# Optimization experiments

Hardware: AMD Instinct MI355X
Metric: run time of the kernel (lower is better)

## Reference

```python
import jax, jax.numpy as jnp
from jax import lax
import numpy as np

BN_EPS = 1e-5

def _bn(x, g, b, m, v):
    # inference-mode BatchNorm1d (running stats)
    return (x - m) * (g / jnp.sqrt(v + BN_EPS)) + b

def _mlp2(x, W1, g, b, m, v, W2):
    # Linear(no bias) -> BN -> ReLU -> (Dropout off in eval) -> Linear(no bias)
    h = jax.nn.relu(_bn(x @ W1.T, g, b, m, v))
    return h @ W2.T

def setup_inputs() -> dict:
    key = jax.random.key(0)
    ks = iter(jax.random.split(key, 40))
    B, N = 1024, 10
    f32 = jnp.float32
    def w(shape, s=0.02):
        return jax.random.normal(next(ks), shape, f32) * s
    def bn_params(c):
        return (jnp.ones((c,), f32), jnp.zeros((c,), f32),
                jax.random.normal(next(ks), (c,), f32) * 0.1,
                jax.random.uniform(next(ks), (c,), f32, 0.5, 1.5))
    inp = {
        'features_object': jax.random.normal(next(ks), (B, N, 1024), f32),
        'bbox': jax.random.uniform(next(ks), (B, N, 4), f32),
        'word_embedding': jax.random.normal(next(ks), (B, N, 300), f32),
        'sentiment': jax.random.normal(next(ks), (B, N, 4096), f32),
        'body': jax.random.normal(next(ks), (B, 2048), f32),
    }
    # mlp_object: 1024 -> 128 -> 128
    inp['W1_o'] = w((128, 1024)); inp['g_o'], inp['b_o'], inp['m_o'], inp['v_o'] = bn_params(128)
    inp['W2_o'] = w((128, 128))
    # mlp_sentiment: 4096 -> 512 -> 128
    inp['W1_s'] = w((512, 4096)); inp['g_s'], inp['b_s'], inp['m_s'], inp['v_s'] = bn_params(512)
    inp['W2_s'] = w((128, 512))
    # mlp_body: 2048 -> 256 -> 128
    inp['W1_b'] = w((256, 2048)); inp['g_b'], inp['b_b'], inp['m_b'], inp['v_b'] = bn_params(256)
    inp['W2_b'] = w((128, 256))
    # channel attention (CBAM-style, in_planes=10, ratio=2): shared MLP 10->5->10
    inp['Wc1'] = w((5, 10), 0.3)
    inp['Wc2'] = w((10, 5), 0.3)
    # spatial attention: Conv1d(2 -> 1, k=7, pad=3, no bias)
    inp['Wsa'] = w((1, 2, 7), 0.3)
    # fc1: 688 -> 256 (with bias) then BN
    inp['Wf'] = w((256, 688)); inp['bf'] = jnp.zeros((256,), f32)
    inp['g_f'], inp['b_f'], inp['m_f'], inp['v_f'] = bn_params(256)
    return inp

def reference(features_object, bbox, word_embedding, sentiment, body,
              W1_o, g_o, b_o, m_o, v_o, W2_o,
              W1_s, g_s, b_s, m_s, v_s, W2_s,
              W1_b, g_b, b_b, m_b, v_b, W2_b,
              Wc1, Wc2, Wsa, Wf, bf, g_f, b_f, m_f, v_f):
    B, N, _ = features_object.shape
    # per-slice MLPs batched into single GEMMs over B*N rows
    obj = _mlp2(features_object.reshape(B * N, -1), W1_o, g_o, b_o, m_o, v_o, W2_o).reshape(B, N, 128)
    sen = _mlp2(sentiment.reshape(B * N, -1), W1_s, g_s, b_s, m_s, v_s, W2_s).reshape(B, N, 128)
    # body is identical across the N repeats (inference BN), compute once and broadcast
    bod = _mlp2(body.reshape(B, -1), W1_b, g_b, b_b, m_b, v_b, W2_b)
    bod = jnp.broadcast_to(bod[:, None, :], (B, N, 128))
    x = jnp.concatenate([obj, bbox, word_embedding, sen, bod], axis=2)  # [B,N,688]
    # channel attention over the N-slice axis
    def ca_mlp(a):  # [B,N] -> [B,N]
        return jax.nn.relu(a @ Wc1.T) @ Wc2.T
    att_c = jax.nn.sigmoid(ca_mlp(x.mean(axis=2)) + ca_mlp(x.max(axis=2)))  # [B,N]
    x = x * att_c[:, :, None]
    # spatial attention along feature axis
    s = jnp.stack([x.mean(axis=1), x.max(axis=1)], axis=1)  # [B,2,688]
    sa = lax.conv_general_dilated(s, Wsa, (1,), [(3, 3)],
                                  dimension_numbers=('NCH', 'OIH', 'NCH'))  # [B,1,688]
    x = x * jax.nn.sigmoid(sa)
    x = x.sum(axis=1)  # [B,688]
    out = jax.nn.relu(_bn(x @ Wf.T + bf, g_f, b_f, m_f, v_f))  # [B,256]
    return out
```

## Files before the change

### kernel.cpp

```cpp
#include <hip/hip_runtime.h>
#include <hip/hip_bf16.h>
#include <math.h>

typedef __attribute__((ext_vector_type(8))) short short8;
typedef __attribute__((ext_vector_type(4))) float floatx4;

static __device__ __forceinline__ unsigned short f2bf(float f) {
    unsigned int u = __float_as_uint(f);
    unsigned int r = (u + 0x7fffu + ((u >> 16) & 1u)) >> 16;
    return (unsigned short)r;
}

static __device__ __forceinline__ unsigned int pk_bf16(float lo, float hi) {
    unsigned int r;
    asm("v_cvt_pk_bf16_f32 %0, %1, %2" : "=v"(r) : "v"(lo), "v"(hi));
    return r;
}

static __device__ __forceinline__ void g2l16(const void* g, void* l) {
    __builtin_amdgcn_global_load_lds(
        (const __attribute__((address_space(1))) unsigned int*)g,
        (__attribute__((address_space(3))) unsigned int*)l,
        16, 0, 0);
}

static __device__ __forceinline__ float4 bnrelu4(float4 v, float4 s, float4 h) {
    float4 r;
    r.x = fmaxf(v.x * s.x + h.x, 0.f);
    r.y = fmaxf(v.y * s.y + h.y, 0.f);
    r.z = fmaxf(v.z * s.z + h.z, 0.f);
    r.w = fmaxf(v.w * s.w + h.w, 0.f);
    return r;
}

struct GDesc {
    const float*          Af;
    const unsigned short* Ab;
    const unsigned short* W;
    float*          Cf;
    unsigned short* Cb;
    const float *bias, *g, *b, *m, *v;
    int M, N, K;
    int Kreal;
    int fuse;
    int nbx;
    int block0;
    int nbb;
    int ksplit;
    int fuseA;
};
struct GArgs { GDesc g[3]; int n; };

__global__ __launch_bounds__(256)
void gemm_grouped(GArgs ga)
{
    __shared__ float          As_f[2][4096];
    __shared__ unsigned short Bs[2][4096];
    __shared__ float scL[256], shL[256];
    unsigned short* As_b = (unsigned short*)&As_f[0][0];

    const int bid = blockIdx.x;
    int gi = 0;
    #pragma unroll
    for (int i = 1; i < 3; ++i)
        if (i < ga.n && bid >= ga.g[i].block0) gi = i;
    const GDesc d = ga.g[gi];

    int local = bid - d.block0;
    {
        const int cpx = (d.nbb * d.ksplit) >> 3;
        local = (local & 7) * cpx + (local >> 3);
    }
    int kc = 0;
    int Kc = d.K;
    if (d.ksplit > 1) {
        Kc = d.K / d.ksplit;
        kc = local / d.nbb;
        local -= kc * d.nbb;
    }
    const int kbeg = kc * Kc;
    const int bx = local % d.nbx;
    const int by = local / d.nbx;
    const int row0 = by * 128;
    const int col0 = bx * 128;

    const int tid  = threadIdx.x;
    const int wave = tid >> 6;
    const int lane = tid & 63;
    const int qd   = lane >> 4;
    const int ln   = lane & 15;
    const int wr   = (wave >> 1) * 64;
    const int wc   = (wave & 1) * 64;

    const int c0 = wave * 128 + lane;
    const int c1 = c0 + 64;
    const int r0 = c0 >> 2, k0 = (((c0 & 3) ^ ((c0 >> 3) & 3))) * 8;
    const int r1 = c1 >> 2, k1 = (((c1 & 3) ^ ((c1 >> 3) & 3))) * 8;

    const int aro  = wave * 32 + (lane >> 3);
    const int acol = ((lane & 7) ^ (lane >> 3)) * 4;

    const bool afp = (d.Af != nullptr);
    const int niter = Kc >> 5;

    floatx4 acc[4][4];
    #pragma unroll
    for (int i = 0; i < 4; ++i)
        #pragma unroll
        for (int j = 0; j < 4; ++j) acc[i][j] = (floatx4){0.f, 0.f, 0.f, 0.f};

    if (d.fuseA) {
        for (int k = tid; k < Kc; k += 256) {
            float sc = d.g[kbeg + k] * rsqrtf(d.v[kbeg + k] + 1e-5f);
            scL[k] = sc;
            shL[k] = d.b[kbeg + k] - d.m[kbeg + k] * sc;
        }
    }
    g2l16(d.W + (size_t)(col0 + r0) * d.K + kbeg + k0, &Bs[0][(size_t)wave * 1024]);
    g2l16(d.W + (size_t)(col0 + r1) * d.K + kbeg + k1, &Bs[0][(size_t)wave * 1024 + 512]);
    if (afp) {
        #pragma unroll
        for (int t = 0; t < 4; ++t)
            g2l16(d.Af + (size_t)(row0 + aro + t * 8) * d.Kreal + kbeg + acol,
                  &As_f[0][(size_t)(wave * 4 + t) * 256]);
    } else {
        g2l16(d.Ab + (size_t)(row0 + r0) * d.K + kbeg + k0, As_b + (size_t)wave * 1024);
        g2l16(d.Ab + (size_t)(row0 + r1) * d.K + kbeg + k1, As_b + (size_t)wave * 1024 + 512);
    }
    __syncthreads();

    int cur = 0;
    for (int it = 0; it < niter; ++it) {
        const int nxt = cur ^ 1;
        const bool pf = (it + 1 < niter);

        if (pf) {
            const int kg = kbeg + (it + 1) * 32;
            g2l16(d.W + (size_t)(col0 + r0) * d.K + kg + k0, &Bs[nxt][(size_t)wave * 1024]);
            g2l16(d.W + (size_t)(col0 + r1) * d.K + kg + k1, &Bs[nxt][(size_t)wave * 1024 + 512]);
            if (afp) {
                #pragma unroll
                for (int t = 0; t < 4; ++t)
                    g2l16(d.Af + (size_t)(row0 + aro + t * 8) * d.Kreal + kg + acol,
                          &As_f[nxt][(size_t)(wave * 4 + t) * 256]);
            } else {
                g2l16(d.Ab + (size_t)(row0 + r0) * d.K + kg + k0, As_b + (size_t)nxt * 4096 + wave * 1024);
                g2l16(d.Ab + (size_t)(row0 + r1) * d.K + kg + k1, As_b + (size_t)nxt * 4096 + wave * 1024 + 512);
            }
        }

        short8 a[4], b[4];
        if (afp) {
            const int kl = it * 32;
            #pragma unroll
            for (int i = 0; i < 4; ++i) {
                const int row = wr + i * 16 + ln;
                const int sw  = row & 7;
                const int c0f = ((qd * 2)     ^ sw) * 4;
                const int c1f = ((qd * 2 + 1) ^ sw) * 4;
                float4 v0 = *(const float4*)&As_f[cur][row * 32 + c0f];
                float4 v1 = *(const float4*)&As_f[cur][row * 32 + c1f];
                if (d.fuseA) {
                    const int kf = kl + qd * 8;
                    v0 = bnrelu4(v0, *(const float4*)&scL[kf],
                                     *(const float4*)&shL[kf]);
                    v1 = bnrelu4(v1, *(const float4*)&scL[kf + 4],
                                     *(const float4*)&shL[kf + 4]);
                }
                int4 pk = { (int)pk_bf16(v0.x, v0.y), (int)pk_bf16(v0.z, v0.w),
                            (int)pk_bf16(v1.x, v1.y), (int)pk_bf16(v1.z, v1.w) };
                a[i] = *(short8*)&pk;
            }
        } else {
            #pragma unroll
            for (int i = 0; i < 4; ++i) {
                const int row = wr + i * 16 + ln;
                const int sw  = (row >> 1) & 3;
                a[i] = *(const short8*)&As_b[(size_t)cur * 4096 + row * 32 + (qd ^ sw) * 8];
            }
        }
        #pragma unroll
        for (int j = 0; j < 4; ++j) {
            const int row = wc + j * 16 + ln;
            const int sw  = (row >> 1) & 3;
            b[j] = *(const short8*)&Bs[cur][row * 32 + (qd ^ sw) * 8];
        }
        #pragma unroll
        for (int i = 0; i < 4; ++i)
            #pragma unroll
            for (int j = 0; j < 4; ++j)
                acc[i][j] = __builtin_amdgcn_mfma_f32_16x16x32_bf16(
                                a[i], b[j], acc[i][j], 0, 0, 0);

        __syncthreads();
        cur = nxt;
    }

    if (d.ksplit > 1) {
        #pragma unroll
        for (int j = 0; j < 4; ++j) {
            const int col = col0 + wc + j * 16 + ln;
            #pragma unroll
            for (int i = 0; i < 4; ++i) {
                #pragma unroll
                for (int r = 0; r < 4; ++r) {
                    const int row = row0 + wr + i * 16 + qd * 4 + r;
                    atomicAdd(&d.Cf[(size_t)row * d.N + col], acc[i][j][r]);
                }
            }
        }
        return;
    }

    #pragma unroll
    for (int j = 0; j < 4; ++j) {
        const int col = col0 + wc + j * 16 + ln;
        float add = d.bias ? d.bias[col] : 0.f;
        float scale = 1.f, shift = 0.f;
        if (d.fuse) {
            scale = d.g[col] * rsqrtf(d.v[col] + 1e-5f);
            shift = d.b[col] - d.m[col] * scale;
        }
        #pragma unroll
        for (int i = 0; i < 4; ++i) {
            #pragma unroll
            for (int r = 0; r < 4; ++r) {
                const int row = row0 + wr + i * 16 + qd * 4 + r;
                float vv = acc[i][j][r] + add;
                if (d.fuse) vv = fmaxf(vv * scale + shift, 0.f);
                if (d.Cf) d.Cf[(size_t)row * d.N + col] = vv;
                if (d.Cb) d.Cb[(size_t)row * d.N + col] = f2bf(vv);
            }
        }
    }
}

struct WSeg { const float* src; void* dst; int Kreal; int Kp; };
struct WArgs { WSeg s[7]; int off[8]; float4* zdst; int zn; };

__global__ __launch_bounds__(256)
void cvt_weights(WArgs wa)
{
    int i = blockIdx.x * 256 + threadIdx.x;
    if (i >= wa.off[7]) {
        int z = i - wa.off[7];
        if (z < wa.zn) wa.zdst[z] = (float4){0.f, 0.f, 0.f, 0.f};
        return;
    }
    int s = 0;
    #pragma unroll
    for (int j = 1; j < 7; ++j) if (i >= wa.off[j]) s = j;
    const WSeg sg = wa.s[s];
    const int li = i - wa.off[s];
    if (s == 6) {
        const int k2 = li >> 8, c = li & 255;
        const int ka = k2 * 2, kb = k2 * 2 + 1;
        unsigned int lo = (ka < 688) ? f2bf(sg.src[(size_t)c * 688 + ka]) : 0u;
        unsigned int hi = (kb < 688) ? f2bf(sg.src[(size_t)c * 688 + kb]) : 0u;
        ((unsigned int*)sg.dst)[li] = lo | (hi << 16);
        return;
    }
    const int r = li / sg.Kp, c = li - r * sg.Kp;
    ((unsigned short*)sg.dst)[li] =
        (c < sg.Kreal) ? f2bf(sg.src[(size_t)r * sg.Kreal + c]) : (unsigned short)0;
}

__global__ __launch_bounds__(256)
void attn_kernel(const float* __restrict__ obj, const float* __restrict__ bbox,
                 const float* __restrict__ word, const float* __restrict__ sen,
                 const float* __restrict__ bod,
                 const float* __restrict__ Wc1, const float* __restrict__ Wc2,
                 const float* __restrict__ Wsa,
                 const unsigned int* __restrict__ wfpk,
                 const float* __restrict__ bf,
                 const float* __restrict__ g_f, const float* __restrict__ b_f,
                 const float* __restrict__ m_f, const float* __restrict__ v_f,
                 float* __restrict__ out)
{
    const int b = blockIdx.x;
    const int tid = threadIdx.x;

    __shared__ float xs[10][688];
    __shared__ float s0[688], s1[688];
    __shared__ float xr[688];
    __shared__ float avec[10], mvec[10], att[10];
    __shared__ float cw[14], c1[50], c2[50];

    if (tid < 14) cw[tid] = Wsa[tid];
    if (tid < 50) { c1[tid] = Wc1[tid]; c2[tid] = Wc2[tid]; }

    for (int n = 0; n < 10; ++n) {
        const float* o  = obj  + ((size_t)b * 10 + n) * 128;
        const float* bx = bbox + ((size_t)b * 10 + n) * 4;
        const float* w  = word + ((size_t)b * 10 + n) * 300;
        const float* s  = sen  + ((size_t)b * 10 + n) * 128;
        const float* bo = bod  + (size_t)b * 128;
        for (int c = tid; c < 688; c += 256) {
            float v;
            if      (c < 128) v = o[c];
            else if (c < 132) v = bx[c - 128];
            else if (c < 432) v = w[c - 132];
            else if (c < 560) v = s[c - 432];
            else              v = bo[c - 560];
            xs[n][c] = v;
        }
    }
    __syncthreads();

    {
        const int wv = tid >> 6, ln2 = tid & 63;
        for (int n = wv; n < 10; n += 4) {
            float sm = 0.f, mx = -INFINITY;
            for (int c = ln2; c < 688; c += 64) {
                float v = xs[n][c];
                sm += v; mx = fmaxf(mx, v);
            }
            #pragma unroll
            for (int off = 32; off > 0; off >>= 1) {
                sm += __shfl_down(sm, off);
                mx = fmaxf(mx, __shfl_down(mx, off));
            }
            if (ln2 == 0) { avec[n] = sm * (1.f / 688.f); mvec[n] = mx; }
        }
    }
    __syncthreads();

    if (tid == 0) {
        float ha[5], hm[5];
        #pragma unroll
        for (int i = 0; i < 5; ++i) {
            float sa_ = 0.f, sm_ = 0.f;
            #pragma unroll
            for (int j = 0; j < 10; ++j) {
                sa_ += c1[i * 10 + j] * avec[j];
                sm_ += c1[i * 10 + j] * mvec[j];
            }
            ha[i] = fmaxf(sa_, 0.f);
            hm[i] = fmaxf(sm_, 0.f);
        }
        #pragma unroll
        for (int j = 0; j < 10; ++j) {
            float v = 0.f;
            #pragma unroll
            for (int i = 0; i < 5; ++i) v += c2[j * 5 + i] * (ha[i] + hm[i]);
            att[j] = 1.f / (1.f + expf(-v));
        }
    }
    __syncthreads();

    for (int c = tid; c < 688; c += 256) {
        float sm = 0.f, mx = -INFINITY;
        #pragma unroll
        for (int n = 0; n < 10; ++n) {
            float v = xs[n][c] * att[n];
            xs[n][c] = v;
            sm += v; mx = fmaxf(mx, v);
        }
        s0[c] = sm * 0.1f;
        s1[c] = mx;
    }
    __syncthreads();

    for (int c = tid; c < 688; c += 256) {
        float sa = 0.f;
        #pragma unroll
        for (int j = 0; j < 7; ++j) {
            int cc = c + j - 3;
            if (cc >= 0 && cc < 688)
                sa += cw[j] * s0[cc] + cw[7 + j] * s1[cc];
        }
        float sig = 1.f / (1.f + expf(-sa));
        float sm = 0.f;
        #pragma unroll
        for (int n = 0; n < 10; ++n) sm += xs[n][c];
        xr[c] = sm * sig;
    }
    __syncthreads();

    {
        float acc = 0.f;
        #pragma unroll 4
        for (int k2 = 0; k2 < 344; ++k2) {
            unsigned int w2 = wfpk[(size_t)k2 * 256 + tid];
            float wlo = __uint_as_float(w2 << 16);
            float whi = __uint_as_float(w2 & 0xffff0000u);
            acc += wlo * xr[2 * k2] + whi * xr[2 * k2 + 1];
        }
        float sc = g_f[tid] * rsqrtf(v_f[tid] + 1e-5f);
        float sh = b_f[tid] - m_f[tid] * sc;
        out[(size_t)b * 256 + tid] = fmaxf((acc + bf[tid]) * sc + sh, 0.f);
    }
}

extern "C" void kernel_launch(void* const* d_in, const int* in_sizes, int n_in,
                              void* d_out, int out_size, void* d_ws, size_t ws_size,
                              hipStream_t stream)
{
    const float* f_obj = (const float*)d_in[0];
    const float* bbox  = (const float*)d_in[1];
    const float* word  = (const float*)d_in[2];
    const float* sent  = (const float*)d_in[3];
    const float* body  = (const float*)d_in[4];
    const float* W1_o  = (const float*)d_in[5];
    const float* g_o = (const float*)d_in[6],  *b_o = (const float*)d_in[7];
    const float* m_o = (const float*)d_in[8],  *v_o = (const float*)d_in[9];
    const float* W2_o  = (const float*)d_in[10];
    const float* W1_s  = (const float*)d_in[11];
    const float* g_s = (const float*)d_in[12], *b_s = (const float*)d_in[13];
    const float* m_s = (const float*)d_in[14], *v_s = (const float*)d_in[15];
    const float* W2_s  = (const float*)d_in[16];
    const float* W1_b  = (const float*)d_in[17];
    const float* g_b = (const float*)d_in[18], *b_b = (const float*)d_in[19];
    const float* m_b = (const float*)d_in[20], *v_b = (const float*)d_in[21];
    const float* W2_b  = (const float*)d_in[22];
    const float* Wc1 = (const float*)d_in[23];
    const float* Wc2 = (const float*)d_in[24];
    const float* Wsa = (const float*)d_in[25];
    const float* Wf  = (const float*)d_in[26];
    const float* bf  = (const float*)d_in[27];
    const float* g_f = (const float*)d_in[28], *b_f = (const float*)d_in[29];
    const float* m_f = (const float*)d_in[30], *v_f = (const float*)d_in[31];
    float* out = (float*)d_out;

    char* p = (char*)d_ws;
    unsigned short* w1s  = (unsigned short*)p; p += 4194304;
    unsigned short* w2s  = (unsigned short*)p; p += 131072;
    unsigned short* w1o  = (unsigned short*)p; p += 262144;
    unsigned short* w2o  = (unsigned short*)p; p += 32768;
    unsigned short* w1b  = (unsigned short*)p; p += 1048576;
    unsigned short* w2b  = (unsigned short*)p; p += 65536;
    unsigned int*   wfpk = (unsigned int*)p;   p += 360448;
    char* zbase = p;
    float* sen_f = (float*)p; p += 5242880;
    float* obj_f = (float*)p; p += 5242880;
    float* bod_f = (float*)p; p += 524288;
    float* ps    = (float*)p; p += 20971520;
    float* po    = (float*)p; p += 5242880;
    float* pb    = (float*)p; p += 1048576;
    const int zbytes = 38273024;
    if ((size_t)(p - (char*)d_ws) > ws_size) return;

    WArgs wa;
    wa.s[0] = { W1_s, w1s,  4096, 4096 };
    wa.s[1] = { W2_s, w2s,   512,  512 };
    wa.s[2] = { W1_o, w1o,  1024, 1024 };
    wa.s[3] = { W2_o, w2o,   128,  128 };
    wa.s[4] = { W1_b, w1b,  2048, 2048 };
    wa.s[5] = { W2_b, w2b,   256,  256 };
    wa.s[6] = { Wf,   wfpk,  688,  704 };
    const int wn[7] = { 512*4096, 128*512, 128*1024, 128*128, 256*2048, 128*256, 352*256 };
    wa.off[0] = 0;
    for (int i = 0; i < 7; ++i) wa.off[i + 1] = wa.off[i] + wn[i];
    wa.zdst = (float4*)zbase;
    wa.zn   = zbytes / 16;
    cvt_weights<<<(wa.off[7] + wa.zn + 255) / 256, 256, 0, stream>>>(wa);

    {
        GArgs ga; ga.n = 3;
        ga.g[0] = { sent,  nullptr, w1s, ps, nullptr, nullptr, nullptr, nullptr, nullptr, nullptr,
                    10240, 512, 4096, 4096, 0, 4, 0,   320, 2, 0 };
        ga.g[1] = { f_obj, nullptr, w1o, po, nullptr, nullptr, nullptr, nullptr, nullptr, nullptr,
                    10240, 128, 1024, 1024, 0, 1, 640, 80,  2, 0 };
        ga.g[2] = { body,  nullptr, w1b, pb, nullptr, nullptr, nullptr, nullptr, nullptr, nullptr,
                    1024,  256, 2048, 2048, 0, 2, 800, 16,  2, 0 };
        gemm_grouped<<<832, 256, 0, stream>>>(ga);
    }

    {
        GArgs ga; ga.n = 3;
        ga.g[0] = { ps, nullptr, w2s, sen_f, nullptr, nullptr, g_s, b_s, m_s, v_s,
                    10240, 128, 512, 512, 0, 1, 0,   80, 2, 1 };
        ga.g[1] = { po, nullptr, w2o, obj_f, nullptr, nullptr, g_o, b_o, m_o, v_o,
                    10240, 128, 128, 128, 0, 1, 160, 80, 2, 1 };
        ga.g[2] = { pb, nullptr, w2b, bod_f, nullptr, nullptr, g_b, b_b, m_b, v_b,
                    1024,  128, 256, 256, 0, 1, 320, 8,  2, 1 };
        gemm_grouped<<<336, 256, 0, stream>>>(ga);
    }

    attn_kernel<<<1024, 256, 0, stream>>>(obj_f, bbox, word, sen_f, bod_f,
                                          Wc1, Wc2, Wsa, wfpk, bf,
                                          g_f, b_f, m_f, v_f, out);
}
```

Baseline: 495.5 us.

## Fuse second MLP layers with BN/ReLU into attention kernel

The second-layer GEMMs for the sentiment, object and body branches, with their BN+ReLU on the hidden activations, move into the per-batch attention kernel. There they run as scalar FMA loops over packed bf16 weights and bf16 hidden values held in shared memory. This removes one grouped GEMM launch and the fp32 intermediate round-trip (sen_f/obj_f/bod_f), and shrinks the zeroed workspace. In exchange the attention kernel does about 128x(512+128) MACs per row on CUDA cores instead of MFMA, and its shared-memory use rises, which may lower occupancy. The GEMM kernel is simplified to the split-K atomic path only.

Measured after the change: 561.6 us. +13.3%, slower.

```diff
diff --git a/kernel.cpp b/kernel.cpp
--- a/kernel.cpp
+++ b/kernel.cpp
@@ -24,30 +24,16 @@
         16, 0, 0);
 }
 
-static __device__ __forceinline__ float4 bnrelu4(float4 v, float4 s, float4 h) {
-    float4 r;
-    r.x = fmaxf(v.x * s.x + h.x, 0.f);
-    r.y = fmaxf(v.y * s.y + h.y, 0.f);
-    r.z = fmaxf(v.z * s.z + h.z, 0.f);
-    r.w = fmaxf(v.w * s.w + h.w, 0.f);
-    return r;
-}
-
 struct GDesc {
     const float*          Af;
-    const unsigned short* Ab;
     const unsigned short* W;
     float*          Cf;
-    unsigned short* Cb;
-    const float *bias, *g, *b, *m, *v;
     int M, N, K;
     int Kreal;
-    int fuse;
     int nbx;
     int block0;
     int nbb;
     int ksplit;
-    int fuseA;
 };
 struct GArgs { GDesc g[3]; int n; };
 
@@ -56,8 +42,6 @@
 {
     __shared__ float          As_f[2][4096];
     __shared__ unsigned short Bs[2][4096];
-    __shared__ float scL[256], shL[256];
-    unsigned short* As_b = (unsigned short*)&As_f[0][0];
 
     const int bid = blockIdx.x;
     int gi = 0;
@@ -100,7 +84,6 @@
     const int aro  = wave * 32 + (lane >> 3);
     const int acol = ((lane & 7) ^ (lane >> 3)) * 4;
 
-    const bool afp = (d.Af != nullptr);
     const int niter = Kc >> 5;
 
     floatx4 acc[4][4];
@@ -109,24 +92,12 @@
         #pragma unroll
         for (int j = 0; j < 4; ++j) acc[i][j] = (floatx4){0.f, 0.f, 0.f, 0.f};
 
-    if (d.fuseA) {
-        for (int k = tid; k < Kc; k += 256) {
-            float sc = d.g[kbeg + k] * rsqrtf(d.v[kbeg + k] + 1e-5f);
-            scL[k] = sc;
-            shL[k] = d.b[kbeg + k] - d.m[kbeg + k] * sc;
-        }
-    }
     g2l16(d.W + (size_t)(col0 + r0) * d.K + kbeg + k0, &Bs[0][(size_t)wave * 1024]);
     g2l16(d.W + (size_t)(col0 + r1) * d.K + kbeg + k1, &Bs[0][(size_t)wave * 1024 + 512]);
-    if (afp) {
-        #pragma unroll
-        for (int t = 0; t < 4; ++t)
-            g2l16(d.Af + (size_t)(row0 + aro + t * 8) * d.Kreal + kbeg + acol,
-                  &As_f[0][(size_t)(wave * 4 + t) * 256]);
-    } else {
-        g2l16(d.Ab + (size_t)(row0 + r0) * d.K + kbeg + k0, As_b + (size_t)wave * 1024);
-        g2l16(d.Ab + (size_t)(row0 + r1) * d.K + kbeg + k1, As_b + (size_t)wave * 1024 + 512);
-    }
+    #pragma unroll
+    for (int t = 0; t < 4; ++t)
+        g2l16(d.Af + (size_t)(row0 + aro + t * 8) * d.Kreal + kbeg + acol,
+              &As_f[0][(size_t)(wave * 4 + t) * 256]);
     __syncthreads();
 
     int cur = 0;
@@ -138,46 +109,22 @@
             const int kg = kbeg + (it + 1) * 32;
             g2l16(d.W + (size_t)(col0 + r0) * d.K + kg + k0, &Bs[nxt][(size_t)wave * 1024]);
             g2l16(d.W + (size_t)(col0 + r1) * d.K + kg + k1, &Bs[nxt][(size_t)wave * 1024 + 512]);
-            if (afp) {
-                #pragma unroll
-                for (int t = 0; t < 4; ++t)
-                    g2l16(d.Af + (size_t)(row0 + aro + t * 8) * d.Kreal + kg + acol,
-                          &As_f[nxt][(size_t)(wave * 4 + t) * 256]);
-            } else {
-                g2l16(d.Ab + (size_t)(row0 + r0) * d.K + kg + k0, As_b + (size_t)nxt * 4096 + wave * 1024);
-                g2l16(d.Ab + (size_t)(row0 + r1) * d.K + kg + k1, As_b + (size_t)nxt * 4096 + wave * 1024 + 512);
-            }
+            #pragma unroll
+            for (int t = 0; t < 4; ++t)
+                g2l16(d.Af + (size_t)(row0 + aro + t * 8) * d.Kreal + kg + acol,
+                      &As_f[nxt][(size_t)(wave * 4 + t) * 256]);
         }
 
         short8 a[4], b[4];
-        if (afp) {
-            const int kl = it * 32;
-            #pragma unroll
-            for (int i = 0; i < 4; ++i) {
-                const int row = wr + i * 16 + ln;
-                const int sw  = row & 7;
-                const int c0f = ((qd * 2)     ^ sw) * 4;
-                const int c1f = ((qd * 2 + 1) ^ sw) * 4;
-                float4 v0 = *(const float4*)&As_f[cur][row * 32 + c0f];
-                float4 v1 = *(const float4*)&As_f[cur][row * 32 + c1f];
-                if (d.fuseA) {
-                    const int kf = kl + qd * 8;
-                    v0 = bnrelu4(v0, *(const float4*)&scL[kf],
-                                     *(const float4*)&shL[kf]);
-                    v1 = bnrelu4(v1, *(const float4*)&scL[kf + 4],
-                                     *(const float4*)&shL[kf + 4]);
-                }
-                int4 pk = { (int)pk_bf16(v0.x, v0.y), (int)pk_bf16(v0.z, v0.w),
-                            (int)pk_bf16(v1.x, v1.y), (int)pk_bf16(v1.z, v1.w) };
-                a[i] = *(short8*)&pk;
-            }
-        } else {
-            #pragma unroll
-            for (int i = 0; i < 4; ++i) {
-                const int row = wr + i * 16 + ln;
-                const int sw  = (row >> 1) & 3;
-                a[i] = *(const short8*)&As_b[(size_t)cur * 4096 + row * 32 + (qd ^ sw) * 8];
-            }
+        #pragma unroll
+        for (int i = 0; i < 4; ++i) {
+            const int row = wr + i * 16 + ln;
+            const int sw  = row & 7;
+            float4 v0 = *(const float4*)&As_f[cur][row * 32 + ((qd * 2)     ^ sw) * 4];
+            float4 v1 = *(const float4*)&As_f[cur][row * 32 + ((qd * 2 + 1) ^ sw) * 4];
+            int4 pk = { (int)pk_bf16(v0.x, v0.y), (int)pk_bf16(v0.z, v0.w),
+                        (int)pk_bf16(v1.x, v1.y), (int)pk_bf16(v1.z, v1.w) };
+            a[i] = *(short8*)&pk;
         }
         #pragma unroll
         for (int j = 0; j < 4; ++j) {
@@ -196,46 +143,21 @@
         cur = nxt;
     }
 
-    if (d.ksplit > 1) {
-        #pragma unroll
-        for (int j = 0; j < 4; ++j) {
-            const int col = col0 + wc + j * 16 + ln;
-            #pragma unroll
-            for (int i = 0; i < 4; ++i) {
-                #pragma unroll
-                for (int r = 0; r < 4; ++r) {
-                    const int row = row0 + wr + i * 16 + qd * 4 + r;
-                    atomicAdd(&d.Cf[(size_t)row * d.N + col], acc[i][j][r]);
-                }
-            }
-        }
-        return;
-    }
-
     #pragma unroll
     for (int j = 0; j < 4; ++j) {
         const int col = col0 + wc + j * 16 + ln;
-        float add = d.bias ? d.bias[col] : 0.f;
-        float scale = 1.f, shift = 0.f;
-        if (d.fuse) {
-            scale = d.g[col] * rsqrtf(d.v[col] + 1e-5f);
-            shift = d.b[col] - d.m[col] * scale;
-        }
         #pragma unroll
         for (int i = 0; i < 4; ++i) {
             #pragma unroll
             for (int r = 0; r < 4; ++r) {
                 const int row = row0 + wr + i * 16 + qd * 4 + r;
-                float vv = acc[i][j][r] + add;
-                if (d.fuse) vv = fmaxf(vv * scale + shift, 0.f);
-                if (d.Cf) d.Cf[(size_t)row * d.N + col] = vv;
-                if (d.Cb) d.Cb[(size_t)row * d.N + col] = f2bf(vv);
-            }
-        }
-    }
-}
-
-struct WSeg { const float* src; void* dst; int Kreal; int Kp; };
+                atomicAdd(&d.Cf[(size_t)row * d.N + col], acc[i][j][r]);
+            }
+        }
+    }
+}
+
+struct WSeg { const float* src; void* dst; int Kreal; int Kp; int packed; int nlog; };
 struct WArgs { WSeg s[7]; int off[8]; float4* zdst; int zn; };
 
 __global__ __launch_bounds__(256)
@@ -252,11 +174,12 @@
     for (int j = 1; j < 7; ++j) if (i >= wa.off[j]) s = j;
     const WSeg sg = wa.s[s];
     const int li = i - wa.off[s];
-    if (s == 6) {
-        const int k2 = li >> 8, c = li & 255;
-        const int ka = k2 * 2, kb = k2 * 2 + 1;
-        unsigned int lo = (ka < 688) ? f2bf(sg.src[(size_t)c * 688 + ka]) : 0u;
-        unsigned int hi = (kb < 688) ? f2bf(sg.src[(size_t)c * 688 + kb]) : 0u;
+    if (sg.packed) {
+        const int c  = li & ((1 << sg.nlog) - 1);
+        const int k2 = li >> sg.nlog;
+        const int ka = 2 * k2, kb = ka + 1;
+        unsigned int lo = (ka < sg.Kreal) ? f2bf(sg.src[(size_t)c * sg.Kreal + ka]) : 0u;
+        unsigned int hi = (kb < sg.Kreal) ? f2bf(sg.src[(size_t)c * sg.Kreal + kb]) : 0u;
         ((unsigned int*)sg.dst)[li] = lo | (hi << 16);
         return;
     }
@@ -265,45 +188,120 @@
         (c < sg.Kreal) ? f2bf(sg.src[(size_t)r * sg.Kreal + c]) : (unsigned short)0;
 }
 
+struct AArgs {
+    const float *ps, *po, *pb, *bbox, *word;
+    const unsigned int *w2s, *w2o, *w2b, *wf;
+    const float *g_s, *b_s, *m_s, *v_s;
+    const float *g_o, *b_o, *m_o, *v_o;
+    const float *g_b, *b_b, *m_b, *v_b;
+    const float *Wc1, *Wc2, *Wsa, *bf;
+    const float *g_f, *b_f, *m_f, *v_f;
+    float* out;
+};
+
+static __device__ __forceinline__ unsigned int bnpair(
+    const float* src, const float* g, const float* bb,
+    const float* m, const float* v, int k2)
+{
+    float2 a = *(const float2*)(src + 2 * k2);
+    float sc0 = g[2 * k2]     * rsqrtf(v[2 * k2]     + 1e-5f);
+    float sc1 = g[2 * k2 + 1] * rsqrtf(v[2 * k2 + 1] + 1e-5f);
+    float h0 = fmaxf(a.x * sc0 + (bb[2 * k2]     - m[2 * k2]     * sc0), 0.f);
+    float h1 = fmaxf(a.y * sc1 + (bb[2 * k2 + 1] - m[2 * k2 + 1] * sc1), 0.f);
+    return pk_bf16(h0, h1);
+}
+
 __global__ __launch_bounds__(256)
-void attn_kernel(const float* __restrict__ obj, const float* __restrict__ bbox,
-                 const float* __restrict__ word, const float* __restrict__ sen,
-                 const float* __restrict__ bod,
-                 const float* __restrict__ Wc1, const float* __restrict__ Wc2,
-                 const float* __restrict__ Wsa,
-                 const unsigned int* __restrict__ wfpk,
-                 const float* __restrict__ bf,
-                 const float* __restrict__ g_f, const float* __restrict__ b_f,
-                 const float* __restrict__ m_f, const float* __restrict__ v_f,
-                 float* __restrict__ out)
+void attn_kernel(AArgs aa)
 {
     const int b = blockIdx.x;
     const int tid = threadIdx.x;
 
     __shared__ float xs[10][688];
-    __shared__ float s0[688], s1[688];
-    __shared__ float xr[688];
+    __shared__ float s0[688], s1[688], xr[688];
+    __shared__ unsigned int h1p[10][256];
+    __shared__ float bodv[128];
     __shared__ float avec[10], mvec[10], att[10];
     __shared__ float cw[14], c1[50], c2[50];
 
-    if (tid < 14) cw[tid] = Wsa[tid];
-    if (tid < 50) { c1[tid] = Wc1[tid]; c2[tid] = Wc2[tid]; }
+    if (tid < 14) cw[tid] = aa.Wsa[tid];
+    if (tid < 50) { c1[tid] = aa.Wc1[tid]; c2[tid] = aa.Wc2[tid]; }
 
     for (int n = 0; n < 10; ++n) {
-        const float* o  = obj  + ((size_t)b * 10 + n) * 128;
-        const float* bx = bbox + ((size_t)b * 10 + n) * 4;
-        const float* w  = word + ((size_t)b * 10 + n) * 300;
-        const float* s  = sen  + ((size_t)b * 10 + n) * 128;
-        const float* bo = bod  + (size_t)b * 128;
-        for (int c = tid; c < 688; c += 256) {
-            float v;
-            if      (c < 128) v = o[c];
-            else if (c < 132) v = bx[c - 128];
-            else if (c < 432) v = w[c - 132];
-            else if (c < 560) v = s[c - 432];
-            else              v = bo[c - 560];
-            xs[n][c] = v;
-        }
+        const float* bx = aa.bbox + ((size_t)b * 10 + n) * 4;
+        const float* w  = aa.word + ((size_t)b * 10 + n) * 300;
+        for (int c = tid; c < 304; c += 256)
+            xs[n][128 + c] = (c < 4) ? bx[c] : w[c - 4];
+    }
+
+    for (int i = tid; i < 2560; i += 256) {
+        const int n = i >> 8, k2 = i & 255;
+        h1p[n][k2] = bnpair(aa.ps + ((size_t)b * 10 + n) * 512,
+                            aa.g_s, aa.b_s, aa.m_s, aa.v_s, k2);
+    }
+    __syncthreads();
+    {
+        const int j = tid & 127, n0 = tid >> 7;
+        float acc[5] = {0.f, 0.f, 0.f, 0.f, 0.f};
+        for (int k2 = 0; k2 < 256; ++k2) {
+            const unsigned int wv = aa.w2s[k2 * 128 + j];
+            const float wlo = __uint_as_float(wv << 16);
+            const float whi = __uint_as_float(wv & 0xffff0000u);
+            #pragma unroll
+            for (int t = 0; t < 5; ++t) {
+                const unsigned int hv = h1p[n0 + 2 * t][k2];
+                acc[t] += wlo * __uint_as_float(hv << 16)
+                        + whi * __uint_as_float(hv & 0xffff0000u);
+            }
+        }
+        __syncthreads();
+        #pragma unroll
+        for (int t = 0; t < 5; ++t) xs[n0 + 2 * t][432 + j] = acc[t];
+    }
+
+    for (int i = tid; i < 640; i += 256) {
+        const int n = i >> 6, k2 = i & 63;
+        h1p[n][k2] = bnpair(aa.po + ((size_t)b * 10 + n) * 128,
+                            aa.g_o, aa.b_o, aa.m_o, aa.v_o, k2);
+    }
+    __syncthreads();
+    {
+        const int j = tid & 127, n0 = tid >> 7;
+        float acc[5] = {0.f, 0.f, 0.f, 0.f, 0.f};
+        for (int k2 = 0; k2 < 64; ++k2) {
+            const unsigned int wv = aa.w2o[k2 * 128 + j];
+            const float wlo = __uint_as_float(wv << 16);
+            const float whi = __uint_as_float(wv & 0xffff0000u);
+            #pragma unroll
+            for (int t = 0; t < 5; ++t) {
+                const unsigned int hv = h1p[n0 + 2 * t][k2];
+                acc[t] += wlo * __uint_as_float(hv << 16)
+                        + whi * __uint_as_float(hv & 0xffff0000u);
+            }
+        }
+        __syncthreads();
+        #pragma unroll
+        for (int t = 0; t < 5; ++t) xs[n0 + 2 * t][j] = acc[t];
+    }
+
+    if (tid < 128)
+        h1p[0][tid] = bnpair(aa.pb + (size_t)b * 256,
+                             aa.g_b, aa.b_b, aa.m_b, aa.v_b, tid);
+    __syncthreads();
+    if (tid < 128) {
+        float acc = 0.f;
+        for (int k2 = 0; k2 < 128; ++k2) {
+            const unsigned int wv = aa.w2b[k2 * 128 + tid];
+            const unsigned int hv = h1p[0][k2];
+            acc += __uint_as_float(wv << 16) * __uint_as_float(hv << 16)
+                 + __uint_as_float(wv & 0xffff0000u) * __uint_as_float(hv & 0xffff0000u);
+        }
+        bodv[tid] = acc;
+    }
+    __syncthreads();
+    for (int i = tid; i < 1280; i += 256) {
+        const int n = i >> 7, j = i & 127;
+        xs[n][560 + j] = bodv[j];
     }
     __syncthreads();
 
@@ -381,14 +379,13 @@
         float acc = 0.f;
         #pragma unroll 4
         for (int k2 = 0; k2 < 344; ++k2) {
-            unsigned int w2 = wfpk[(size_t)k2 * 256 + tid];
-            float wlo = __uint_as_float(w2 << 16);
-            float whi = __uint_as_float(w2 & 0xffff0000u);
-            acc += wlo * xr[2 * k2] + whi * xr[2 * k2 + 1];
-        }
-        float sc = g_f[tid] * rsqrtf(v_f[tid] + 1e-5f);
-        float sh = b_f[tid] - m_f[tid] * sc;
-        out[(size_t)b * 256 + tid] = fmaxf((acc + bf[tid]) * sc + sh, 0.f);
+            unsigned int w2 = aa.wf[(size_t)k2 * 256 + tid];
+            acc += __uint_as_float(w2 << 16)         * xr[2 * k2]
+                 + __uint_as_float(w2 & 0xffff0000u) * xr[2 * k2 + 1];
+        }
+        float sc = aa.g_f[tid] * rsqrtf(aa.v_f[tid] + 1e-5f);
+        float sh = aa.b_f[tid] - aa.m_f[tid] * sc;
+        aa.out[(size_t)b * 256 + tid] = fmaxf((acc + aa.bf[tid]) * sc + sh, 0.f);
     }
 }
 
@@ -424,31 +421,28 @@
 
     char* p = (char*)d_ws;
     unsigned short* w1s  = (unsigned short*)p; p += 4194304;
-    unsigned short* w2s  = (unsigned short*)p; p += 131072;
     unsigned short* w1o  = (unsigned short*)p; p += 262144;
-    unsigned short* w2o  = (unsigned short*)p; p += 32768;
     unsigned short* w1b  = (unsigned short*)p; p += 1048576;
-    unsigned short* w2b  = (unsigned short*)p; p += 65536;
+    unsigned int*   w2sp = (unsigned int*)p;   p += 131072;
+    unsigned int*   w2op = (unsigned int*)p;   p += 32768;
+    unsigned int*   w2bp = (unsigned int*)p;   p += 65536;
     unsigned int*   wfpk = (unsigned int*)p;   p += 360448;
     char* zbase = p;
-    float* sen_f = (float*)p; p += 5242880;
-    float* obj_f = (float*)p; p += 5242880;
-    float* bod_f = (float*)p; p += 524288;
-    float* ps    = (float*)p; p += 20971520;
-    float* po    = (float*)p; p += 5242880;
-    float* pb    = (float*)p; p += 1048576;
-    const int zbytes = 38273024;
+    float* ps = (float*)p; p += 20971520;
+    float* po = (float*)p; p += 5242880;
+    float* pb = (float*)p; p += 1048576;
+    const int zbytes = 27262976;
     if ((size_t)(p - (char*)d_ws) > ws_size) return;
 
     WArgs wa;
-    wa.s[0] = { W1_s, w1s,  4096, 4096 };
-    wa.s[1] = { W2_s, w2s,   512,  512 };
-    wa.s[2] = { W1_o, w1o,  1024, 1024 };
-    wa.s[3] = { W2_o, w2o,   128,  128 };
-    wa.s[4] = { W1_b, w1b,  2048, 2048 };
-    wa.s[5] = { W2_b, w2b,   256,  256 };
-    wa.s[6] = { Wf,   wfpk,  688,  704 };
-    const int wn[7] = { 512*4096, 128*512, 128*1024, 128*128, 256*2048, 128*256, 352*256 };
+    wa.s[0] = { W1_s, w1s,  4096, 4096, 0, 0 };
+    wa.s[1] = { W1_o, w1o,  1024, 1024, 0, 0 };
+    wa.s[2] = { W1_b, w1b,  2048, 2048, 0, 0 };
+    wa.s[3] = { W2_s, w2sp,  512, 0,    1, 7 };
+    wa.s[4] = { W2_o, w2op,  128, 0,    1, 7 };
+    wa.s[5] = { W2_b, w2bp,  256, 0,    1, 7 };
+    wa.s[6] = { Wf,   wfpk,  688, 0,    1, 8 };
+    const int wn[7] = { 512*4096, 128*1024, 256*2048, 32768, 8192, 16384, 90112 };
     wa.off[0] = 0;
     for (int i = 0; i < 7; ++i) wa.off[i + 1] = wa.off[i] + wn[i];
     wa.zdst = (float4*)zbase;
@@ -457,27 +451,22 @@
 
     {
         GArgs ga; ga.n = 3;
-        ga.g[0] = { sent,  nullptr, w1s, ps, nullptr, nullptr, nullptr, nullptr, nullptr, nullptr,
-                    10240, 512, 4096, 4096, 0, 4, 0,   320, 2, 0 };
-        ga.g[1] = { f_obj, nullptr, w1o, po, nullptr, nullptr, nullptr, nullptr, nullptr, nullptr,
-                    10240, 128, 1024, 1024, 0, 1, 640, 80,  2, 0 };
-        ga.g[2] = { body,  nullptr, w1b, pb, nullptr, nullptr, nullptr, nullptr, nullptr, nullptr,
-                    1024,  256, 2048, 2048, 0, 2, 800, 16,  2, 0 };
+        ga.g[0] = { sent,  w1s, ps, 10240, 512, 4096, 4096, 4, 0,   320, 2 };
+        ga.g[1] = { f_obj, w1o, po, 10240, 128, 1024, 1024, 1, 640, 80,  2 };
+        ga.g[2] = { body,  w1b, pb, 1024,  256, 2048, 2048, 2, 800, 16,  2 };
         gemm_grouped<<<832, 256, 0, stream>>>(ga);
     }
 
     {
-        GArgs ga; ga.n = 3;
-        ga.g[0] = { ps, nullptr, w2s, sen_f, nullptr, nullptr, g_s, b_s, m_s, v_s,
-                    10240, 128, 512, 512, 0, 1, 0,   80, 2, 1 };
-        ga.g[1] = { po, nullptr, w2o, obj_f, nullptr, nullptr, g_o, b_o, m_o, v_o,
-                    10240, 128, 128, 128, 0, 1, 160, 80, 2, 1 };
-        ga.g[2] = { pb, nullptr, w2b, bod_f, nullptr, nullptr, g_b, b_b, m_b, v_b,
-                    1024,  128, 256, 256, 0, 1, 320, 8,  2, 1 };
-        gemm_grouped<<<336, 256, 0, stream>>>(ga);
-    }
-
-    attn_kernel<<<1024, 256, 0, stream>>>(obj_f, bbox, word, sen_f, bod_f,
-                                          Wc1, Wc2, Wsa, wfpk, bf,
-                                          g_f, b_f, m_f, v_f, out);
-}
+        AArgs aa;
+        aa.ps = ps; aa.po = po; aa.pb = pb; aa.bbox = bbox; aa.word = word;
+        aa.w2s = w2sp; aa.w2o = w2op; aa.w2b = w2bp; aa.wf = wfpk;
+        aa.g_s = g_s; aa.b_s = b_s; aa.m_s = m_s; aa.v_s = v_s;
+        aa.g_o = g_o; aa.b_o = b_o; aa.m_o = m_o; aa.v_o = v_o;
+        aa.g_b = g_b; aa.b_b = b_b; aa.m_b = m_b; aa.v_b = v_b;
+        aa.Wc1 = Wc1; aa.Wc2 = Wc2; aa.Wsa = Wsa; aa.bf = bf;
+        aa.g_f = g_f; aa.b_f = b_f; aa.m_f = m_f; aa.v_f = v_f;
+        aa.out = out;
+        attn_kernel<<<1024, 256, 0, stream>>>(aa);
+    }
+}
```
